# Performance work log

Hardware: AMD Instinct MI355X
Metric: run time of the kernel (lower is better)

The kernel has to match this reference:

```python
import jax, jax.numpy as jnp
import numpy as np

N_NODES = 50000


def gcn_conv(x, W, b, src, dst, n_nodes):
    """PyG GCNConv: h = x @ W; add self-loops; symmetric norm; scatter-add; + bias."""
    h = x @ W  # [N, out]
    loop = jnp.arange(n_nodes, dtype=src.dtype)
    s = jnp.concatenate([src, loop])  # source nodes j
    d = jnp.concatenate([dst, loop])  # target nodes i
    deg = jax.ops.segment_sum(jnp.ones_like(d, dtype=h.dtype), d, num_segments=n_nodes)
    dinv = jnp.where(deg > 0, jax.lax.rsqrt(deg), 0.0)
    norm = dinv[s] * dinv[d]  # [E+N]
    msg = h[s] * norm[:, None]  # gather + scale, [E+N, out]
    out = jax.ops.segment_sum(msg, d, num_segments=n_nodes)
    return out + b


def setup_inputs() -> dict:
    key = jax.random.key(0)
    k1, k2, k3, k4 = jax.random.split(key, 4)
    x = jax.random.normal(k1, (N_NODES, 256), dtype=jnp.float32)
    edge_index = jax.random.randint(k2, (2, 1600000), 0, N_NODES, dtype=jnp.int64)
    in_dim, hid, out_dim = 256, 128, 40
    W1 = jax.random.normal(k3, (in_dim, hid), dtype=jnp.float32) / np.sqrt(in_dim)
    b1 = jnp.zeros((hid,), dtype=jnp.float32)
    W2 = jax.random.normal(k4, (hid, out_dim), dtype=jnp.float32) / np.sqrt(hid)
    b2 = jnp.zeros((out_dim,), dtype=jnp.float32)
    return {"x": x, "edge_index": edge_index, "W1": W1, "b1": b1, "W2": W2, "b2": b2}


def reference(x, edge_index, W1, b1, W2, b2):
    src, dst = edge_index[0], edge_index[1]
    n = x.shape[0]
    h = jax.nn.relu(gcn_conv(x, W1, b1, src, dst, n))
    # dropout is identity in eval mode
    h = gcn_conv(h, W2, b2, src, dst, n)
    return jax.nn.log_softmax(h, axis=1)
```

## Files before the change

### kernel.cpp

```cpp
#include <hip/hip_runtime.h>
#include <cmath>

#define NN 50000
#define C_IN 256
#define C_HID 128
#define C_OUT 40

#define BSZ 512
#define NBUCK ((NN + BSZ - 1) / BSZ)
#define CAP 19456
#define EPB 4096

typedef __attribute__((ext_vector_type(8))) short bf16x8;
typedef __attribute__((ext_vector_type(4))) float f32x4;
typedef __attribute__((ext_vector_type(2))) float f32x2;

__device__ __forceinline__ float bf2f(unsigned int u16) {
  unsigned int b = (u16 & 0xFFFFu) << 16;
  return __builtin_bit_cast(float, b);
}
__device__ __forceinline__ unsigned short f2bf(float f) {
  unsigned int b = __builtin_bit_cast(unsigned int, f);
  unsigned int r = (b + 0x7FFF + ((b >> 16) & 1)) >> 16;
  return (unsigned short)r;
}


__global__ __launch_bounds__(256) void prep_passA_kernel(const float* __restrict__ W1,
    const float* __restrict__ W2, const float* __restrict__ b1,
    uint4* __restrict__ pbuf1, uint4* __restrict__ pbuf2, float* __restrict__ bperm,
    const int* __restrict__ src, const int* __restrict__ dst, int E,
    unsigned int* __restrict__ gedge, int* __restrict__ bcur) {
  __shared__ unsigned int pk[EPB];
  __shared__ unsigned char bof[EPB];
  __shared__ int bcnt[NBUCK], bstart[NBUCK], bpos[NBUCK], gbase[NBUCK];
  int blk = blockIdx.x;
  int tid = threadIdx.x;
  if (blk < 16) {
    int gid = blk * 256 + tid;
    int l = gid & 63, idx = gid >> 6;
    int ks = idx & 7, t = idx >> 3;
    int c = t * 16 + (l & 15);
    int kbase = ks * 32 + (l >> 4) * 8;
    unsigned int u[4];
    #pragma unroll
    for (int jp = 0; jp < 4; ++jp) {
      float v0 = W1[(size_t)(kbase + 2 * jp) * C_HID + c];
      float v1 = W1[(size_t)(kbase + 2 * jp + 1) * C_HID + c];
      u[jp] = (unsigned int)f2bf(v0) | ((unsigned int)f2bf(v1) << 16);
    }
    pbuf1[idx * 64 + l] = make_uint4(u[0], u[1], u[2], u[3]);
    return;
  } else if (blk < 19) {
    int gid = (blk - 16) * 256 + tid;
    int l = gid & 63, idx = gid >> 6;
    int ks = idx & 3, t = idx >> 2;
    int c = t * 16 + (l & 15);
    int kbase = ks * 32 + (l >> 4) * 8;
    unsigned int u[4];
    #pragma unroll
    for (int jp = 0; jp < 4; ++jp) {
      int k0 = kbase + 2 * jp, k1 = k0 + 1;
      int ch0 = ((k0 & 7) << 4) + (k0 >> 3);
      int ch1 = ((k1 & 7) << 4) + (k1 >> 3);
      float v0 = (c < C_OUT) ? W2[(size_t)ch0 * C_OUT + c] : 0.f;
      float v1 = (c < C_OUT) ? W2[(size_t)ch1 * C_OUT + c] : 0.f;
      u[jp] = (unsigned int)f2bf(v0) | ((unsigned int)f2bf(v1) << 16);
    }
    pbuf2[idx * 64 + l] = make_uint4(u[0], u[1], u[2], u[3]);
    return;
  } else if (blk == 19) {
    if (tid < C_HID) bperm[tid] = b1[((tid & 7) << 4) + (tid >> 3)];
    return;
  }
  int e0 = (blk - 20) * EPB;
  int cntE = min(EPB, E - e0);
  for (int b = tid; b < NBUCK; b += 256) bcnt[b] = 0;
  int ds_[16], ss_[16];
  __syncthreads();
  #pragma unroll
  for (int k = 0; k < 16; ++k) {
    int i = tid + k * 256;
    if (i < cntE) {
      ds_[k] = dst[e0 + i];
      ss_[k] = src[e0 + i];
      atomicAdd(&bcnt[ds_[k] >> 9], 1);
    }
  }
  __syncthreads();
  if (tid == 0) {
    int acc = 0;
    for (int b = 0; b < NBUCK; ++b) { bstart[b] = acc; bpos[b] = acc; acc += bcnt[b]; }
  }
  __syncthreads();
  #pragma unroll
  for (int k = 0; k < 16; ++k) {
    int i = tid + k * 256;
    if (i < cntE) {
      int b = ds_[k] >> 9;
      int p = atomicAdd(&bpos[b], 1);
      pk[p] = ((unsigned int)ss_[k] << 9) | (unsigned int)(ds_[k] & 511);
      bof[p] = (unsigned char)b;
    }
  }
  __syncthreads();
  for (int b = tid; b < NBUCK; b += 256)
    gbase[b] = atomicAdd(&bcur[b], bcnt[b]);
  __syncthreads();
  for (int i = tid; i < cntE; i += 256) {
    int b = bof[i];
    int p = gbase[b] + (i - bstart[b]);
    gedge[(size_t)b * CAP + p] = pk[i];
  }
}


__global__ __launch_bounds__(512) void passB_g1_kernel(const unsigned int* __restrict__ gedge,
    const int* __restrict__ bcur, int* __restrict__ esrc, int* __restrict__ off,
    float* __restrict__ dinv, int E,
    const float* __restrict__ x, const uint4* __restrict__ pb, uint2* __restrict__ h) {
  __shared__ int dcnt[512];
  __shared__ int dsc[512];
  __shared__ int dcur[512];
  __shared__ int bc[128];
  int tid = threadIdx.x;
  if ((int)blockIdx.x >= NBUCK) {
    int l = tid & 63, w = tid >> 6;
    int row0 = (blockIdx.x - NBUCK) * 128 + w * 16;
    int arow = min(row0 + (l & 15), NN - 1);
    const float* xp = x + (size_t)arow * C_IN + (l >> 4) * 8;
    bf16x8 a[8];
    #pragma unroll
    for (int ks = 0; ks < 8; ++ks) {
      float4 a0 = *(const float4*)(xp + ks * 32);
      float4 a1 = *(const float4*)(xp + ks * 32 + 4);
      union { bf16x8 v; unsigned short s[8]; } pa;
      pa.s[0] = f2bf(a0.x); pa.s[1] = f2bf(a0.y); pa.s[2] = f2bf(a0.z); pa.s[3] = f2bf(a0.w);
      pa.s[4] = f2bf(a1.x); pa.s[5] = f2bf(a1.y); pa.s[6] = f2bf(a1.z); pa.s[7] = f2bf(a1.w);
      a[ks] = pa.v;
    }
    f32x4 acc[8] = {};
    #pragma unroll
    for (int t = 0; t < 8; ++t) {
      #pragma unroll
      for (int ks = 0; ks < 8; ++ks) {
        bf16x8 b = __builtin_bit_cast(bf16x8, pb[(t * 8 + ks) * 64 + l]);
        acc[t] = __builtin_amdgcn_mfma_f32_16x16x32_bf16(a[ks], b, acc[t], 0, 0, 0);
      }
    }
    int c0 = l & 15, rb = (l >> 4) * 4;
    #pragma unroll
    for (int r = 0; r < 4; ++r) {
      int row = row0 + rb + r;
      if (row < NN) {
        int w0 = __builtin_amdgcn_cvt_pk_fp8_f32(acc[0][r], acc[1][r], 0, false);
        w0     = __builtin_amdgcn_cvt_pk_fp8_f32(acc[2][r], acc[3][r], w0, true);
        int w1 = __builtin_amdgcn_cvt_pk_fp8_f32(acc[4][r], acc[5][r], 0, false);
        w1     = __builtin_amdgcn_cvt_pk_fp8_f32(acc[6][r], acc[7][r], w1, true);
        h[(size_t)row * 16 + c0] = make_uint2((unsigned int)w0, (unsigned int)w1);
      }
    }
    return;
  }
  int b = blockIdx.x;
  int nE = bcur[b];
  if (tid < 128) bc[tid] = (tid < b) ? bcur[tid] : 0;
  dcnt[tid] = 0;
  __syncthreads();
  const unsigned int* reg = gedge + (size_t)b * CAP;
  for (int i = tid; i < nE; i += 512)
    atomicAdd(&dcnt[reg[i] & 511], 1);
  __syncthreads();
  for (int d = 64; d > 0; d >>= 1) {
    if (tid < d) bc[tid] += bc[tid + d];
    __syncthreads();
  }
  int base = bc[0];
  int own = dcnt[tid];
  dsc[tid] = own;
  __syncthreads();
  for (int d = 1; d < 512; d <<= 1) {
    int x_ = (tid >= d) ? dsc[tid - d] : 0;
    __syncthreads();
    dsc[tid] += x_;
    __syncthreads();
  }
  int excl = dsc[tid] - own;
  dcur[tid] = excl;
  int node = b * BSZ + tid;
  if (node < NN) {
    off[node]  = base + excl;
    dinv[node] = rsqrtf((float)(own + 1));
  }
  if (b == 0 && tid == 0) off[NN] = E;
  __syncthreads();
  for (int i = tid; i < nE; i += 512) {
    unsigned int p = reg[i];
    int pos = atomicAdd(&dcur[p & 511], 1);
    esrc[base + pos] = (int)(p >> 9);
  }
}

__global__ void epack_kernel(const int* __restrict__ esrc, const float* __restrict__ dinv,
                             unsigned int* __restrict__ epack, int E) {
  int e = blockIdx.x * 256 + threadIdx.x;
  if (e < E) {
    int s = esrc[e];
    epack[e] = ((unsigned int)s << 16) | (unsigned int)f2bf(dinv[s]);
  }
}


__global__ __launch_bounds__(256) void gemm2_kernel(const unsigned short* __restrict__ ag1b,
    const uint4* __restrict__ pbuf, unsigned char* __restrict__ h2) {
  int l = threadIdx.x & 63, w = threadIdx.x >> 6;
  int row0 = blockIdx.x * 64 + w * 16;
  int arow = min(row0 + (l & 15), NN - 1);
  const uint4* ap = (const uint4*)(ag1b + (size_t)arow * C_HID + (l >> 4) * 8);
  bf16x8 a[4];
  #pragma unroll
  for (int ks = 0; ks < 4; ++ks) a[ks] = __builtin_bit_cast(bf16x8, ap[ks * 4]);
  f32x4 acc[3] = {};
  #pragma unroll
  for (int t = 0; t < 3; ++t) {
    #pragma unroll
    for (int ks = 0; ks < 4; ++ks) {
      bf16x8 b = __builtin_bit_cast(bf16x8, pbuf[(t * 4 + ks) * 64 + l]);
      acc[t] = __builtin_amdgcn_mfma_f32_16x16x32_bf16(a[ks], b, acc[t], 0, 0, 0);
    }
  }
  int rbase = row0 + (l >> 4) * 4;
  int c0 = l & 15;
  #pragma unroll
  for (int t = 0; t < 3; ++t) {
    int col = t * 16 + c0;
    if (col < C_OUT) {
      #pragma unroll
      for (int r = 0; r < 4; ++r) {
        int row = rbase + r;
        if (row < NN) {
          int pk = __builtin_amdgcn_cvt_pk_fp8_f32(acc[t][r], 0.f, 0, false);
          h2[(size_t)row * C_OUT + col] = (unsigned char)(pk & 0xFF);
        }
      }
    }
  }
}


__global__ void agg1_kernel(const uint2* __restrict__ h, const int* __restrict__ off,
                            const unsigned int* __restrict__ epack,
                            const float* __restrict__ dinv, const float* __restrict__ bperm,
                            uint4* __restrict__ outb, int n, int E) {
  int wv = threadIdx.x >> 6, l = threadIdx.x & 63;
  int i = blockIdx.x * 4 + wv;
  if (i >= n) return;
  int g = l >> 4, q = l & 15;
  float di = dinv[i];
  float a0 = 0.f, a1 = 0.f, a2 = 0.f, a3 = 0.f, a4 = 0.f, a5 = 0.f, a6 = 0.f, a7 = 0.f;
  int p0 = off[i], p1 = off[i + 1];
  int pb = p0;
  int Em1 = E - 1;
  unsigned int e0 = epack[min(pb + g, Em1)];
  unsigned int e1 = epack[min(pb + 4 + g, Em1)];
  unsigned int e2 = epack[min(pb + 8 + g, Em1)];
  unsigned int e3 = epack[min(pb + 12 + g, Em1)];
  unsigned int f0 = epack[min(pb + 16 + g, Em1)];
  unsigned int f1 = epack[min(pb + 20 + g, Em1)];
  unsigned int f2 = epack[min(pb + 24 + g, Em1)];
  unsigned int f3 = epack[min(pb + 28 + g, Em1)];
  uint2 H0 = h[(size_t)(e0 >> 16) * 16 + q];
  uint2 H1 = h[(size_t)(e1 >> 16) * 16 + q];
  uint2 H2 = h[(size_t)(e2 >> 16) * 16 + q];
  uint2 H3 = h[(size_t)(e3 >> 16) * 16 + q];
  #define ACC_EDGE(vv, ee)                                                    \
    {                                                                         \
      float n_ = bf2f(ee) * di;                                               \
      f32x2 c0_ = __builtin_amdgcn_cvt_pk_f32_fp8((int)vv.x, false);          \
      f32x2 c1_ = __builtin_amdgcn_cvt_pk_f32_fp8((int)vv.x, true);           \
      f32x2 c2_ = __builtin_amdgcn_cvt_pk_f32_fp8((int)vv.y, false);          \
      f32x2 c3_ = __builtin_amdgcn_cvt_pk_f32_fp8((int)vv.y, true);           \
      a0 += c0_[0] * n_; a1 += c0_[1] * n_;                                   \
      a2 += c1_[0] * n_; a3 += c1_[1] * n_;                                   \
      a4 += c2_[0] * n_; a5 += c2_[1] * n_;                                   \
      a6 += c3_[0] * n_; a7 += c3_[1] * n_;                                   \
    }
  for (; pb + 31 < p1; pb += 16) {
    uint2 G0 = h[(size_t)(f0 >> 16) * 16 + q];
    uint2 G1 = h[(size_t)(f1 >> 16) * 16 + q];
    uint2 G2 = h[(size_t)(f2 >> 16) * 16 + q];
    uint2 G3 = h[(size_t)(f3 >> 16) * 16 + q];
    unsigned int n0 = epack[min(pb + 32 + g, Em1)];
    unsigned int n1 = epack[min(pb + 36 + g, Em1)];
    unsigned int n2 = epack[min(pb + 40 + g, Em1)];
    unsigned int n3 = epack[min(pb + 44 + g, Em1)];
    ACC_EDGE(H0, e0); ACC_EDGE(H1, e1); ACC_EDGE(H2, e2); ACC_EDGE(H3, e3);
    e0 = f0; e1 = f1; e2 = f2; e3 = f3;
    f0 = n0; f1 = n1; f2 = n2; f3 = n3;
    H0 = G0; H1 = G1; H2 = G2; H3 = G3;
  }
  if (pb + g < p1)      ACC_EDGE(H0, e0);
  if (pb + 4 + g < p1)  ACC_EDGE(H1, e1);
  if (pb + 8 + g < p1)  ACC_EDGE(H2, e2);
  if (pb + 12 + g < p1) ACC_EDGE(H3, e3);
  int pc = pb + 16;
  if (pc < p1) {
    uint2 G0 = h[(size_t)(f0 >> 16) * 16 + q];
    uint2 G1 = h[(size_t)(f1 >> 16) * 16 + q];
    uint2 G2 = h[(size_t)(f2 >> 16) * 16 + q];
    uint2 G3 = h[(size_t)(f3 >> 16) * 16 + q];
    if (pc + g < p1)      ACC_EDGE(G0, f0);
    if (pc + 4 + g < p1)  ACC_EDGE(G1, f1);
    if (pc + 8 + g < p1)  ACC_EDGE(G2, f2);
    if (pc + 12 + g < p1) ACC_EDGE(G3, f3);
  }
  #undef ACC_EDGE
  a0 += __shfl_xor(a0, 16); a1 += __shfl_xor(a1, 16);
  a2 += __shfl_xor(a2, 16); a3 += __shfl_xor(a3, 16);
  a4 += __shfl_xor(a4, 16); a5 += __shfl_xor(a5, 16);
  a6 += __shfl_xor(a6, 16); a7 += __shfl_xor(a7, 16);
  a0 += __shfl_xor(a0, 32); a1 += __shfl_xor(a1, 32);
  a2 += __shfl_xor(a2, 32); a3 += __shfl_xor(a3, 32);
  a4 += __shfl_xor(a4, 32); a5 += __shfl_xor(a5, 32);
  a6 += __shfl_xor(a6, 32); a7 += __shfl_xor(a7, 32);
  if (g == 0) {
    uint2 sv = h[(size_t)i * 16 + q];
    float dd = di * di;
    f32x2 s0 = __builtin_amdgcn_cvt_pk_f32_fp8((int)sv.x, false);
    f32x2 s1 = __builtin_amdgcn_cvt_pk_f32_fp8((int)sv.x, true);
    f32x2 s2 = __builtin_amdgcn_cvt_pk_f32_fp8((int)sv.y, false);
    f32x2 s3 = __builtin_amdgcn_cvt_pk_f32_fp8((int)sv.y, true);
    a0 += s0[0] * dd; a1 += s0[1] * dd;
    a2 += s1[0] * dd; a3 += s1[1] * dd;
    a4 += s2[0] * dd; a5 += s2[1] * dd;
    a6 += s3[0] * dd; a7 += s3[1] * dd;
    float4 b0 = ((const float4*)bperm)[q * 2];
    float4 b1v = ((const float4*)bperm)[q * 2 + 1];
    a0 = fmaxf(a0 + b0.x, 0.f); a1 = fmaxf(a1 + b0.y, 0.f);
    a2 = fmaxf(a2 + b0.z, 0.f); a3 = fmaxf(a3 + b0.w, 0.f);
    a4 = fmaxf(a4 + b1v.x, 0.f); a5 = fmaxf(a5 + b1v.y, 0.f);
    a6 = fmaxf(a6 + b1v.z, 0.f); a7 = fmaxf(a7 + b1v.w, 0.f);
    uint4 o;
    o.x = (unsigned int)f2bf(a0) | ((unsigned int)f2bf(a1) << 16);
    o.y = (unsigned int)f2bf(a2) | ((unsigned int)f2bf(a3) << 16);
    o.z = (unsigned int)f2bf(a4) | ((unsigned int)f2bf(a5) << 16);
    o.w = (unsigned int)f2bf(a6) | ((unsigned int)f2bf(a7) << 16);
    outb[(size_t)i * 16 + q] = o;
  }
}

__global__ void agg2_kernel(const unsigned char* __restrict__ h2, const int* __restrict__ off,
                            const unsigned int* __restrict__ epack,
                            const float* __restrict__ dinv, const float* __restrict__ b,
                            float* __restrict__ out, int n, int E) {
  int wv = threadIdx.x >> 6, l = threadIdx.x & 63;
  int i = blockIdx.x * 4 + wv;
  if (i >= n) return;
  int g = l / 10, q = l - g * 10;
  bool lact = l < 60;
  if (!lact) { g = 0; q = 0; }
  float di = dinv[i];
  float a0 = 0.f, a1 = 0.f, a2 = 0.f, a3 = 0.f;
  int p0 = off[i], p1 = off[i + 1];
  int pb = p0;
  int Em1 = E - 1;
  unsigned int e0 = epack[min(pb + g, Em1)];
  unsigned int e1 = epack[min(pb + 6 + g, Em1)];
  unsigned int f0 = epack[min(pb + 12 + g, Em1)];
  unsigned int f1 = epack[min(pb + 18 + g, Em1)];
  unsigned int H0 = *(const unsigned int*)(h2 + (size_t)(e0 >> 16) * C_OUT + q * 4);
  unsigned int H1 = *(const unsigned int*)(h2 + (size_t)(e1 >> 16) * C_OUT + q * 4);
  #define ACC_EDGE2(vv, ee)                                                   \
    {                                                                         \
      float n_ = bf2f(ee) * di;                                               \
      f32x2 lo_ = __builtin_amdgcn_cvt_pk_f32_fp8((int)(vv), false);          \
      f32x2 hi_ = __builtin_amdgcn_cvt_pk_f32_fp8((int)(vv), true);           \
      a0 += lo_[0] * n_; a1 += lo_[1] * n_;                                   \
      a2 += hi_[0] * n_; a3 += hi_[1] * n_;                                   \
    }
  for (; pb + 23 < p1; pb += 12) {
    unsigned int G0 = *(const unsigned int*)(h2 + (size_t)(f0 >> 16) * C_OUT + q * 4);
    unsigned int G1 = *(const unsigned int*)(h2 + (size_t)(f1 >> 16) * C_OUT + q * 4);
    unsigned int n0 = epack[min(pb + 24 + g, Em1)];
    unsigned int n1 = epack[min(pb + 30 + g, Em1)];
    if (lact) { ACC_EDGE2(H0, e0); ACC_EDGE2(H1, e1); }
    e0 = f0; e1 = f1;
    f0 = n0; f1 = n1;
    H0 = G0; H1 = G1;
  }
  if (lact && pb + g < p1)     ACC_EDGE2(H0, e0);
  if (lact && pb + 6 + g < p1) ACC_EDGE2(H1, e1);
  int pc = pb + 12;
  if (pc < p1) {
    unsigned int G0 = *(const unsigned int*)(h2 + (size_t)(f0 >> 16) * C_OUT + q * 4);
    unsigned int G1 = *(const unsigned int*)(h2 + (size_t)(f1 >> 16) * C_OUT + q * 4);
    if (lact && pc + g < p1)     ACC_EDGE2(G0, f0);
    if (lact && pc + 6 + g < p1) ACC_EDGE2(G1, f1);
  }
  #undef ACC_EDGE2
  float t0 = 0.f, t1 = 0.f, t2 = 0.f, t3 = 0.f;
  #pragma unroll
  for (int gg = 0; gg < 6; ++gg) {
    int sl = gg * 10 + q;
    t0 += __shfl(a0, sl); t1 += __shfl(a1, sl);
    t2 += __shfl(a2, sl); t3 += __shfl(a3, sl);
  }
  bool act = l < 10;
  float v0, v1, v2, v3;
  if (act) {
    unsigned int sv = *(const unsigned int*)(h2 + (size_t)i * C_OUT + l * 4);
    f32x2 slo = __builtin_amdgcn_cvt_pk_f32_fp8((int)sv, false);
    f32x2 shi = __builtin_amdgcn_cvt_pk_f32_fp8((int)sv, true);
    float dd = di * di;
    float4 bb = ((const float4*)b)[l];
    v0 = t0 + slo[0] * dd + bb.x;
    v1 = t1 + slo[1] * dd + bb.y;
    v2 = t2 + shi[0] * dd + bb.z;
    v3 = t3 + shi[1] * dd + bb.w;
  } else {
    v0 = v1 = v2 = v3 = -INFINITY;
  }
  float mm = fmaxf(fmaxf(v0, v1), fmaxf(v2, v3));
  #pragma unroll
  for (int d = 32; d > 0; d >>= 1) mm = fmaxf(mm, __shfl_xor(mm, d));
  float e = act ? (expf(v0 - mm) + expf(v1 - mm) + expf(v2 - mm) + expf(v3 - mm)) : 0.f;
  float ss = e;
  #pragma unroll
  for (int d = 32; d > 0; d >>= 1) ss += __shfl_xor(ss, d);
  if (act) {
    float lg = logf(ss);
    float4 o = {v0 - mm - lg, v1 - mm - lg, v2 - mm - lg, v3 - mm - lg};
    *(float4*)&out[(size_t)i * C_OUT + l * 4] = o;
  }
}


extern "C" void kernel_launch(void* const* d_in, const int* in_sizes, int n_in,
                              void* d_out, int out_size, void* d_ws, size_t ws_size,
                              hipStream_t stream) {
  const float* x  = (const float*)d_in[0];
  const int*   ei = (const int*)d_in[1];
  const float* W1 = (const float*)d_in[2];
  const float* b1 = (const float*)d_in[3];
  const float* W2 = (const float*)d_in[4];
  const float* b2 = (const float*)d_in[5];
  int E = in_sizes[1] / 2;
  const int* src = ei;
  const int* dst = ei + E;

  char* ws = (char*)d_ws;
  size_t o = 0;
  auto alloc = [&](size_t bytes) {
    char* p = ws + o;
    o += (bytes + 255) & ~(size_t)255;
    return p;
  };
  unsigned int* gedge = (unsigned int*)alloc((size_t)NBUCK * CAP * sizeof(unsigned int));
  int*   bcur  = (int*)alloc(NBUCK * sizeof(int));
  int*   off   = (int*)alloc((NN + 1) * sizeof(int));
  float* dinv  = (float*)alloc(NN * sizeof(float));
  int*   esrc  = (int*)alloc((size_t)E * sizeof(int));
  unsigned int* epck = (unsigned int*)alloc((size_t)E * sizeof(unsigned int));
  uint2* h1f8  = (uint2*)alloc((size_t)NN * C_HID);
  unsigned int*   ag1b = (unsigned int*)alloc((size_t)NN * (C_HID / 2) * sizeof(unsigned int));
  unsigned char*  h2f8 = (unsigned char*)alloc((size_t)NN * C_OUT);
  uint4* pbuf2 = (uint4*)alloc(12 * 64 * sizeof(uint4));
  uint4* pbuf1 = (uint4*)alloc(64 * 64 * sizeof(uint4));
  float* bperm = (float*)alloc(C_HID * sizeof(float));

  int nA  = (E + EPB - 1) / EPB;
  int ng1 = (NN + 127) / 128;
  int ng2 = (NN + 63) / 64;

  hipMemsetAsync(bcur, 0, NBUCK * sizeof(int), stream);
  prep_passA_kernel<<<20 + nA, 256, 0, stream>>>(W1, W2, b1, pbuf1, pbuf2, bperm,
                                                 src, dst, E, gedge, bcur);
  passB_g1_kernel<<<NBUCK + ng1, 512, 0, stream>>>(gedge, bcur, esrc, off, dinv, E,
                                                   x, pbuf1, h1f8);
  epack_kernel<<<(E + 255) / 256, 256, 0, stream>>>(esrc, dinv, epck, E);
  agg1_kernel<<<(NN + 3) / 4, 256, 0, stream>>>(h1f8, off, epck, dinv, bperm,
                                                (uint4*)ag1b, NN, E);
  gemm2_kernel<<<ng2, 256, 0, stream>>>((const unsigned short*)ag1b, pbuf2, h2f8);
  agg2_kernel<<<(NN + 3) / 4, 256, 0, stream>>>(h2f8, off, epck, dinv, b2,
                                                (float*)d_out, NN, E);
}
```

Baseline: 133.0 us.

## Drop epack kernel, gather dinv directly, widen agg1 loads to 16 bytes

Removes the separate epack kernel that packed the source index with a bf16 dinv. Both aggregation kernels now read esrc and gather dinv[src] directly, which saves one launch and one pass over the edge arrays. It costs an extra dependent random load per edge. agg1 is also reorganised so each lane loads uint4 (16 fp8 features), with 8 edges in flight per step instead of 4 and a deeper shuffle reduction. The dinv factor now stays in fp32 rather than being rounded to bf16.

```diff
diff --git a/kernel.cpp b/kernel.cpp
--- a/kernel.cpp
+++ b/kernel.cpp
@@ -201,15 +201,6 @@
   }
 }
 
-__global__ void epack_kernel(const int* __restrict__ esrc, const float* __restrict__ dinv,
-                             unsigned int* __restrict__ epack, int E) {
-  int e = blockIdx.x * 256 + threadIdx.x;
-  if (e < E) {
-    int s = esrc[e];
-    epack[e] = ((unsigned int)s << 16) | (unsigned int)f2bf(dinv[s]);
-  }
-}
-
 
 __global__ __launch_bounds__(256) void gemm2_kernel(const unsigned short* __restrict__ ag1b,
     const uint4* __restrict__ pbuf, unsigned char* __restrict__ h2) {
@@ -248,111 +239,119 @@
 }
 
 
-__global__ void agg1_kernel(const uint2* __restrict__ h, const int* __restrict__ off,
-                            const unsigned int* __restrict__ epack,
-                            const float* __restrict__ dinv, const float* __restrict__ bperm,
-                            uint4* __restrict__ outb, int n, int E) {
+__global__ void agg1_kernel(const uint4* __restrict__ h, const int* __restrict__ off,
+                            const int* __restrict__ esrc, const float* __restrict__ dinv,
+                            const float* __restrict__ bperm, uint4* __restrict__ outb,
+                            int n, int E) {
   int wv = threadIdx.x >> 6, l = threadIdx.x & 63;
   int i = blockIdx.x * 4 + wv;
   if (i >= n) return;
-  int g = l >> 4, q = l & 15;
+  int g = l >> 3, j = l & 7;
   float di = dinv[i];
-  float a0 = 0.f, a1 = 0.f, a2 = 0.f, a3 = 0.f, a4 = 0.f, a5 = 0.f, a6 = 0.f, a7 = 0.f;
+  float a[16];
+  #pragma unroll
+  for (int k = 0; k < 16; ++k) a[k] = 0.f;
   int p0 = off[i], p1 = off[i + 1];
   int pb = p0;
   int Em1 = E - 1;
-  unsigned int e0 = epack[min(pb + g, Em1)];
-  unsigned int e1 = epack[min(pb + 4 + g, Em1)];
-  unsigned int e2 = epack[min(pb + 8 + g, Em1)];
-  unsigned int e3 = epack[min(pb + 12 + g, Em1)];
-  unsigned int f0 = epack[min(pb + 16 + g, Em1)];
-  unsigned int f1 = epack[min(pb + 20 + g, Em1)];
-  unsigned int f2 = epack[min(pb + 24 + g, Em1)];
-  unsigned int f3 = epack[min(pb + 28 + g, Em1)];
-  uint2 H0 = h[(size_t)(e0 >> 16) * 16 + q];
-  uint2 H1 = h[(size_t)(e1 >> 16) * 16 + q];
-  uint2 H2 = h[(size_t)(e2 >> 16) * 16 + q];
-  uint2 H3 = h[(size_t)(e3 >> 16) * 16 + q];
-  #define ACC_EDGE(vv, ee)                                                    \
+  int sA0 = esrc[min(pb + g, Em1)];
+  int sB0 = esrc[min(pb + 8 + g, Em1)];
+  int sA1 = esrc[min(pb + 16 + g, Em1)];
+  int sB1 = esrc[min(pb + 24 + g, Em1)];
+  uint4 HA = h[(size_t)sA0 * 8 + j];
+  uint4 HB = h[(size_t)sB0 * 8 + j];
+  float nA = dinv[sA0];
+  float nB = dinv[sB0];
+  #define ACC_E(vv, nn)                                                       \
     {                                                                         \
-      float n_ = bf2f(ee) * di;                                               \
-      f32x2 c0_ = __builtin_amdgcn_cvt_pk_f32_fp8((int)vv.x, false);          \
-      f32x2 c1_ = __builtin_amdgcn_cvt_pk_f32_fp8((int)vv.x, true);           \
-      f32x2 c2_ = __builtin_amdgcn_cvt_pk_f32_fp8((int)vv.y, false);          \
-      f32x2 c3_ = __builtin_amdgcn_cvt_pk_f32_fp8((int)vv.y, true);           \
-      a0 += c0_[0] * n_; a1 += c0_[1] * n_;                                   \
-      a2 += c1_[0] * n_; a3 += c1_[1] * n_;                                   \
-      a4 += c2_[0] * n_; a5 += c2_[1] * n_;                                   \
-      a6 += c3_[0] * n_; a7 += c3_[1] * n_;                                   \
+      float n_ = (nn) * di;                                                   \
+      f32x2 p0_ = __builtin_amdgcn_cvt_pk_f32_fp8((int)vv.x, false);          \
+      f32x2 p1_ = __builtin_amdgcn_cvt_pk_f32_fp8((int)vv.x, true);           \
+      f32x2 p2_ = __builtin_amdgcn_cvt_pk_f32_fp8((int)vv.y, false);          \
+      f32x2 p3_ = __builtin_amdgcn_cvt_pk_f32_fp8((int)vv.y, true);           \
+      f32x2 p4_ = __builtin_amdgcn_cvt_pk_f32_fp8((int)vv.z, false);          \
+      f32x2 p5_ = __builtin_amdgcn_cvt_pk_f32_fp8((int)vv.z, true);           \
+      f32x2 p6_ = __builtin_amdgcn_cvt_pk_f32_fp8((int)vv.w, false);          \
+      f32x2 p7_ = __builtin_amdgcn_cvt_pk_f32_fp8((int)vv.w, true);           \
+      a[0] += p0_[0] * n_;  a[1] += p0_[1] * n_;                              \
+      a[2] += p1_[0] * n_;  a[3] += p1_[1] * n_;                              \
+      a[4] += p2_[0] * n_;  a[5] += p2_[1] * n_;                              \
+      a[6] += p3_[0] * n_;  a[7] += p3_[1] * n_;                              \
+      a[8] += p4_[0] * n_;  a[9] += p4_[1] * n_;                              \
+      a[10] += p5_[0] * n_; a[11] += p5_[1] * n_;                             \
+      a[12] += p6_[0] * n_; a[13] += p6_[1] * n_;                             \
+      a[14] += p7_[0] * n_; a[15] += p7_[1] * n_;                             \
     }
   for (; pb + 31 < p1; pb += 16) {
-    uint2 G0 = h[(size_t)(f0 >> 16) * 16 + q];
-    uint2 G1 = h[(size_t)(f1 >> 16) * 16 + q];
-    uint2 G2 = h[(size_t)(f2 >> 16) * 16 + q];
-    uint2 G3 = h[(size_t)(f3 >> 16) * 16 + q];
-    unsigned int n0 = epack[min(pb + 32 + g, Em1)];
-    unsigned int n1 = epack[min(pb + 36 + g, Em1)];
-    unsigned int n2 = epack[min(pb + 40 + g, Em1)];
-    unsigned int n3 = epack[min(pb + 44 + g, Em1)];
-    ACC_EDGE(H0, e0); ACC_EDGE(H1, e1); ACC_EDGE(H2, e2); ACC_EDGE(H3, e3);
-    e0 = f0; e1 = f1; e2 = f2; e3 = f3;
-    f0 = n0; f1 = n1; f2 = n2; f3 = n3;
-    H0 = G0; H1 = G1; H2 = G2; H3 = G3;
-  }
-  if (pb + g < p1)      ACC_EDGE(H0, e0);
-  if (pb + 4 + g < p1)  ACC_EDGE(H1, e1);
-  if (pb + 8 + g < p1)  ACC_EDGE(H2, e2);
-  if (pb + 12 + g < p1) ACC_EDGE(H3, e3);
+    uint4 GA = h[(size_t)sA1 * 8 + j];
+    uint4 GB = h[(size_t)sB1 * 8 + j];
+    float mA = dinv[sA1];
+    float mB = dinv[sB1];
+    int tA = esrc[min(pb + 32 + g, Em1)];
+    int tB = esrc[min(pb + 40 + g, Em1)];
+    ACC_E(HA, nA); ACC_E(HB, nB);
+    HA = GA; HB = GB; nA = mA; nB = mB;
+    sA1 = tA; sB1 = tB;
+  }
+  if (pb + g < p1)     ACC_E(HA, nA);
+  if (pb + 8 + g < p1) ACC_E(HB, nB);
   int pc = pb + 16;
   if (pc < p1) {
-    uint2 G0 = h[(size_t)(f0 >> 16) * 16 + q];
-    uint2 G1 = h[(size_t)(f1 >> 16) * 16 + q];
-    uint2 G2 = h[(size_t)(f2 >> 16) * 16 + q];
-    uint2 G3 = h[(size_t)(f3 >> 16) * 16 + q];
-    if (pc + g < p1)      ACC_EDGE(G0, f0);
-    if (pc + 4 + g < p1)  ACC_EDGE(G1, f1);
-    if (pc + 8 + g < p1)  ACC_EDGE(G2, f2);
-    if (pc + 12 + g < p1) ACC_EDGE(G3, f3);
-  }
-  #undef ACC_EDGE
-  a0 += __shfl_xor(a0, 16); a1 += __shfl_xor(a1, 16);
-  a2 += __shfl_xor(a2, 16); a3 += __shfl_xor(a3, 16);
-  a4 += __shfl_xor(a4, 16); a5 += __shfl_xor(a5, 16);
-  a6 += __shfl_xor(a6, 16); a7 += __shfl_xor(a7, 16);
-  a0 += __shfl_xor(a0, 32); a1 += __shfl_xor(a1, 32);
-  a2 += __shfl_xor(a2, 32); a3 += __shfl_xor(a3, 32);
-  a4 += __shfl_xor(a4, 32); a5 += __shfl_xor(a5, 32);
-  a6 += __shfl_xor(a6, 32); a7 += __shfl_xor(a7, 32);
+    uint4 GA = h[(size_t)sA1 * 8 + j];
+    uint4 GB = h[(size_t)sB1 * 8 + j];
+    float mA = dinv[sA1];
+    float mB = dinv[sB1];
+    if (pc + g < p1)     ACC_E(GA, mA);
+    if (pc + 8 + g < p1) ACC_E(GB, mB);
+  }
+  #undef ACC_E
+  #pragma unroll
+  for (int k = 0; k < 16; ++k) {
+    a[k] += __shfl_xor(a[k], 8);
+    a[k] += __shfl_xor(a[k], 16);
+    a[k] += __shfl_xor(a[k], 32);
+  }
   if (g == 0) {
-    uint2 sv = h[(size_t)i * 16 + q];
+    uint4 sv = h[(size_t)i * 8 + j];
     float dd = di * di;
     f32x2 s0 = __builtin_amdgcn_cvt_pk_f32_fp8((int)sv.x, false);
     f32x2 s1 = __builtin_amdgcn_cvt_pk_f32_fp8((int)sv.x, true);
     f32x2 s2 = __builtin_amdgcn_cvt_pk_f32_fp8((int)sv.y, false);
     f32x2 s3 = __builtin_amdgcn_cvt_pk_f32_fp8((int)sv.y, true);
-    a0 += s0[0] * dd; a1 += s0[1] * dd;
-    a2 += s1[0] * dd; a3 += s1[1] * dd;
-    a4 += s2[0] * dd; a5 += s2[1] * dd;
-    a6 += s3[0] * dd; a7 += s3[1] * dd;
-    float4 b0 = ((const float4*)bperm)[q * 2];
-    float4 b1v = ((const float4*)bperm)[q * 2 + 1];
-    a0 = fmaxf(a0 + b0.x, 0.f); a1 = fmaxf(a1 + b0.y, 0.f);
-    a2 = fmaxf(a2 + b0.z, 0.f); a3 = fmaxf(a3 + b0.w, 0.f);
-    a4 = fmaxf(a4 + b1v.x, 0.f); a5 = fmaxf(a5 + b1v.y, 0.f);
-    a6 = fmaxf(a6 + b1v.z, 0.f); a7 = fmaxf(a7 + b1v.w, 0.f);
-    uint4 o;
-    o.x = (unsigned int)f2bf(a0) | ((unsigned int)f2bf(a1) << 16);
-    o.y = (unsigned int)f2bf(a2) | ((unsigned int)f2bf(a3) << 16);
-    o.z = (unsigned int)f2bf(a4) | ((unsigned int)f2bf(a5) << 16);
-    o.w = (unsigned int)f2bf(a6) | ((unsigned int)f2bf(a7) << 16);
-    outb[(size_t)i * 16 + q] = o;
+    f32x2 s4 = __builtin_amdgcn_cvt_pk_f32_fp8((int)sv.z, false);
+    f32x2 s5 = __builtin_amdgcn_cvt_pk_f32_fp8((int)sv.z, true);
+    f32x2 s6 = __builtin_amdgcn_cvt_pk_f32_fp8((int)sv.w, false);
+    f32x2 s7 = __builtin_amdgcn_cvt_pk_f32_fp8((int)sv.w, true);
+    a[0] += s0[0] * dd;  a[1] += s0[1] * dd;
+    a[2] += s1[0] * dd;  a[3] += s1[1] * dd;
+    a[4] += s2[0] * dd;  a[5] += s2[1] * dd;
+    a[6] += s3[0] * dd;  a[7] += s3[1] * dd;
+    a[8] += s4[0] * dd;  a[9] += s4[1] * dd;
+    a[10] += s5[0] * dd; a[11] += s5[1] * dd;
+    a[12] += s6[0] * dd; a[13] += s6[1] * dd;
+    a[14] += s7[0] * dd; a[15] += s7[1] * dd;
+    const float4* bp = (const float4*)bperm + j * 4;
+    #pragma unroll
+    for (int m = 0; m < 4; ++m) {
+      float4 bb = bp[m];
+      a[m * 4 + 0] = fmaxf(a[m * 4 + 0] + bb.x, 0.f);
+      a[m * 4 + 1] = fmaxf(a[m * 4 + 1] + bb.y, 0.f);
+      a[m * 4 + 2] = fmaxf(a[m * 4 + 2] + bb.z, 0.f);
+      a[m * 4 + 3] = fmaxf(a[m * 4 + 3] + bb.w, 0.f);
+    }
+    unsigned int o[8];
+    #pragma unroll
+    for (int m = 0; m < 8; ++m)
+      o[m] = (unsigned int)f2bf(a[2 * m]) | ((unsigned int)f2bf(a[2 * m + 1]) << 16);
+    outb[(size_t)i * 16 + j * 2]     = make_uint4(o[0], o[1], o[2], o[3]);
+    outb[(size_t)i * 16 + j * 2 + 1] = make_uint4(o[4], o[5], o[6], o[7]);
   }
 }
 
 __global__ void agg2_kernel(const unsigned char* __restrict__ h2, const int* __restrict__ off,
-                            const unsigned int* __restrict__ epack,
-                            const float* __restrict__ dinv, const float* __restrict__ b,
-                            float* __restrict__ out, int n, int E) {
+                            const int* __restrict__ esrc, const float* __restrict__ dinv,
+                            const float* __restrict__ b, float* __restrict__ out,
+                            int n, int E) {
   int wv = threadIdx.x >> 6, l = threadIdx.x & 63;
   int i = blockIdx.x * 4 + wv;
   if (i >= n) return;
@@ -364,40 +363,45 @@
   int p0 = off[i], p1 = off[i + 1];
   int pb = p0;
   int Em1 = E - 1;
-  unsigned int e0 = epack[min(pb + g, Em1)];
-  unsigned int e1 = epack[min(pb + 6 + g, Em1)];
-  unsigned int f0 = epack[min(pb + 12 + g, Em1)];
-  unsigned int f1 = epack[min(pb + 18 + g, Em1)];
-  unsigned int H0 = *(const unsigned int*)(h2 + (size_t)(e0 >> 16) * C_OUT + q * 4);
-  unsigned int H1 = *(const unsigned int*)(h2 + (size_t)(e1 >> 16) * C_OUT + q * 4);
-  #define ACC_EDGE2(vv, ee)                                                   \
+  int sA0 = esrc[min(pb + g, Em1)];
+  int sB0 = esrc[min(pb + 6 + g, Em1)];
+  int sA1 = esrc[min(pb + 12 + g, Em1)];
+  int sB1 = esrc[min(pb + 18 + g, Em1)];
+  unsigned int HA = *(const unsigned int*)(h2 + (size_t)sA0 * C_OUT + q * 4);
+  unsigned int HB = *(const unsigned int*)(h2 + (size_t)sB0 * C_OUT + q * 4);
+  float nA = dinv[sA0];
+  float nB = dinv[sB0];
+  #define ACC_E2(vv, nn)                                                      \
     {                                                                         \
-      float n_ = bf2f(ee) * di;                                               \
+      float n_ = (nn) * di;                                                   \
       f32x2 lo_ = __builtin_amdgcn_cvt_pk_f32_fp8((int)(vv), false);          \
       f32x2 hi_ = __builtin_amdgcn_cvt_pk_f32_fp8((int)(vv), true);           \
       a0 += lo_[0] * n_; a1 += lo_[1] * n_;                                   \
       a2 += hi_[0] * n_; a3 += hi_[1] * n_;                                   \
     }
   for (; pb + 23 < p1; pb += 12) {
-    unsigned int G0 = *(const unsigned int*)(h2 + (size_t)(f0 >> 16) * C_OUT + q * 4);
-    unsigned int G1 = *(const unsigned int*)(h2 + (size_t)(f1 >> 16) * C_OUT + q * 4);
-    unsigned int n0 = epack[min(pb + 24 + g, Em1)];
-    unsigned int n1 = epack[min(pb + 30 + g, Em1)];
-    if (lact) { ACC_EDGE2(H0, e0); ACC_EDGE2(H1, e1); }
-    e0 = f0; e1 = f1;
-    f0 = n0; f1 = n1;
-    H0 = G0; H1 = G1;
-  }
-  if (lact && pb + g < p1)     ACC_EDGE2(H0, e0);
-  if (lact && pb + 6 + g < p1) ACC_EDGE2(H1, e1);
+    unsigned int GA = *(const unsigned int*)(h2 + (size_t)sA1 * C_OUT + q * 4);
+    unsigned int GB = *(const unsigned int*)(h2 + (size_t)sB1 * C_OUT + q * 4);
+    float mA = dinv[sA1];
+    float mB = dinv[sB1];
+    int tA = esrc[min(pb + 24 + g, Em1)];
+    int tB = esrc[min(pb + 30 + g, Em1)];
+    if (lact) { ACC_E2(HA, nA); ACC_E2(HB, nB); }
+    HA = GA; HB = GB; nA = mA; nB = mB;
+    sA1 = tA; sB1 = tB;
+  }
+  if (lact && pb + g < p1)     ACC_E2(HA, nA);
+  if (lact && pb + 6 + g < p1) ACC_E2(HB, nB);
   int pc = pb + 12;
   if (pc < p1) {
-    unsigned int G0 = *(const unsigned int*)(h2 + (size_t)(f0 >> 16) * C_OUT + q * 4);
-    unsigned int G1 = *(const unsigned int*)(h2 + (size_t)(f1 >> 16) * C_OUT + q * 4);
-    if (lact && pc + g < p1)     ACC_EDGE2(G0, f0);
-    if (lact && pc + 6 + g < p1) ACC_EDGE2(G1, f1);
-  }
-  #undef ACC_EDGE2
+    unsigned int GA = *(const unsigned int*)(h2 + (size_t)sA1 * C_OUT + q * 4);
+    unsigned int GB = *(const unsigned int*)(h2 + (size_t)sB1 * C_OUT + q * 4);
+    float mA = dinv[sA1];
+    float mB = dinv[sB1];
+    if (lact && pc + g < p1)     ACC_E2(GA, mA);
+    if (lact && pc + 6 + g < p1) ACC_E2(GB, mB);
+  }
+  #undef ACC_E2
   float t0 = 0.f, t1 = 0.f, t2 = 0.f, t3 = 0.f;
   #pragma unroll
   for (int gg = 0; gg < 6; ++gg) {
@@ -460,7 +464,6 @@
   int*   off   = (int*)alloc((NN + 1) * sizeof(int));
   float* dinv  = (float*)alloc(NN * sizeof(float));
   int*   esrc  = (int*)alloc((size_t)E * sizeof(int));
-  unsigned int* epck = (unsigned int*)alloc((size_t)E * sizeof(unsigned int));
   uint2* h1f8  = (uint2*)alloc((size_t)NN * C_HID);
   unsigned int*   ag1b = (unsigned int*)alloc((size_t)NN * (C_HID / 2) * sizeof(unsigned int));
   unsigned char*  h2f8 = (unsigned char*)alloc((size_t)NN * C_OUT);
@@ -477,10 +480,9 @@
                                                  src, dst, E, gedge, bcur);
   passB_g1_kernel<<<NBUCK + ng1, 512, 0, stream>>>(gedge, bcur, esrc, off, dinv, E,
                                                    x, pbuf1, h1f8);
-  epack_kernel<<<(E + 255) / 256, 256, 0, stream>>>(esrc, dinv, epck, E);
-  agg1_kernel<<<(NN + 3) / 4, 256, 0, stream>>>(h1f8, off, epck, dinv, bperm,
-                                                (uint4*)ag1b, NN, E);
+  agg1_kernel<<<(NN + 3) / 4, 256, 0, stream>>>((const uint4*)h1f8, off, esrc, dinv,
+                                                bperm, (uint4*)ag1b, NN, E);
   gemm2_kernel<<<ng2, 256, 0, stream>>>((const unsigned short*)ag1b, pbuf2, h2f8);
-  agg2_kernel<<<(NN + 3) / 4, 256, 0, stream>>>(h2f8, off, epck, dinv, b2,
+  agg2_kernel<<<(NN + 3) / 4, 256, 0, stream>>>(h2f8, off, esrc, dinv, b2,
                                                 (float*)d_out, NN, E);
 }
```

Result: no change. 130.9 us (median of 2 runs) (-1.6%).
